# Kernel optimization log

Hardware: AMD Instinct MI355X
Metric: run time of the kernel (lower is better)

The kernel has to match this reference:

```python
import jax, jax.numpy as jnp
import numpy as np

N_NODES = 100000
N_EDGES = 1000000
F_IN = 64
F_HID = 64
F_OUT = 2
NUM_GRAPHS = 64


def setup_inputs() -> dict:
    key = jax.random.key(0)
    ks = jax.random.split(key, 8)
    x = jax.random.normal(ks[0], (N_NODES, F_IN), dtype=jnp.float32)
    edge_index = jax.random.randint(ks[1], (2, N_EDGES), 0, N_NODES, dtype=jnp.int32)
    batch = jnp.sort(jax.random.randint(ks[2], (N_NODES,), 0, NUM_GRAPHS, dtype=jnp.int32))
    s1 = 1.0 / np.sqrt(F_IN)
    s2 = 1.0 / np.sqrt(F_HID)
    W1 = jax.random.normal(ks[3], (F_IN, F_HID), dtype=jnp.float32) * s1
    W2 = jax.random.normal(ks[4], (F_HID, F_HID), dtype=jnp.float32) * s2
    W3 = jax.random.normal(ks[5], (F_HID, F_HID), dtype=jnp.float32) * s2
    Wlin = jax.random.normal(ks[6], (F_HID, F_OUT), dtype=jnp.float32) * s2
    return {
        "x": x, "edge_index": edge_index, "batch": batch,
        "W1": W1, "b1": jnp.zeros((F_HID,), jnp.float32),
        "W2": W2, "b2": jnp.zeros((F_HID,), jnp.float32),
        "W3": W3, "b3": jnp.zeros((F_HID,), jnp.float32),
        "Wlin": Wlin, "blin": jnp.zeros((F_OUT,), jnp.float32),
    }


def _gcn_norm(edge_index, n_nodes):
    # add self-loops, compute symmetric D^-1/2 (A+I) D^-1/2 edge weights
    loops = jnp.arange(n_nodes, dtype=edge_index.dtype)
    src = jnp.concatenate([edge_index[0], loops])  # message source j
    dst = jnp.concatenate([edge_index[1], loops])  # aggregation target i
    deg = jax.ops.segment_sum(jnp.ones_like(dst, dtype=jnp.float32), dst,
                              num_segments=n_nodes)
    dinv = jnp.where(deg > 0, jax.lax.rsqrt(deg), 0.0)
    norm = dinv[src] * dinv[dst]  # [E+N]
    return src, dst, norm


def _gcn_conv(h, W, b, src, dst, norm, n_nodes):
    h = h @ W                                    # [N, F] dense transform first (PyG order)
    msg = h[src] * norm[:, None]                 # gather + scale  [E+N, F]
    agg = jax.ops.segment_sum(msg, dst, num_segments=n_nodes)
    return agg + b


def reference(x, edge_index, batch, W1, b1, W2, b2, W3, b3, Wlin, blin):
    n = x.shape[0]
    src, dst, norm = _gcn_norm(edge_index, n)
    h = jax.nn.relu(_gcn_conv(x, W1, b1, src, dst, norm, n))
    h = jax.nn.relu(_gcn_conv(h, W2, b2, src, dst, norm, n))
    h = _gcn_conv(h, W3, b3, src, dst, norm, n)
    # global mean pool over graphs
    sums = jax.ops.segment_sum(h, batch, num_segments=NUM_GRAPHS)        # [G, F]
    cnts = jax.ops.segment_sum(jnp.ones((n,), jnp.float32), batch,
                               num_segments=NUM_GRAPHS)
    pooled = sums / jnp.maximum(cnts, 1.0)[:, None]
    # dropout(p=0.1) is identity in eval mode
    return pooled @ Wlin + blin
```

## Files before the change

kernel.cpp:

```cpp
#include <hip/hip_runtime.h>

#define FDIM 64

typedef unsigned short u16;

__device__ __forceinline__ u16 f2bf(float x) {
    unsigned int u = __float_as_uint(x);
    return (u16)((u + 0x7fff + ((u >> 16) & 1)) >> 16);
}
__device__ __forceinline__ float bf2f(u16 h) {
    return __uint_as_float(((unsigned int)h) << 16);
}
__device__ __forceinline__ float2 up2(unsigned int u) {
    float2 r;
    r.x = __uint_as_float(u << 16);
    r.y = __uint_as_float(u & 0xffff0000u);
    return r;
}


template <bool BF16IN>
__device__ __forceinline__ void mm_tile64(
    const void* __restrict__ ain, const float* __restrict__ bias, int do_relu,
    u16* __restrict__ t, int n, int blk,
    float (*__restrict__ As)[FDIM + 1], float* __restrict__ Ws)
{
    int tid = threadIdx.x;
    int r0 = blk * 64;

    #pragma unroll
    for (int i = 0; i < 4; ++i) {
        int idx = tid + 256 * i;
        int r = idx >> 4;
        int kq = idx & 15;
        float4 v = make_float4(0.f, 0.f, 0.f, 0.f);
        int R = r0 + r;
        if (R < n) {
            if (BF16IN) {
                ushort4 h = ((const ushort4*)ain)[(size_t)R * 16 + kq];
                v.x = bf2f(h.x); v.y = bf2f(h.y); v.z = bf2f(h.z); v.w = bf2f(h.w);
            } else {
                v = ((const float4*)ain)[(size_t)R * 16 + kq];
            }
            if (bias != nullptr) {
                float4 b = ((const float4*)bias)[kq];
                v.x += b.x; v.y += b.y; v.z += b.z; v.w += b.w;
            }
            if (do_relu) {
                v.x = fmaxf(v.x, 0.f); v.y = fmaxf(v.y, 0.f);
                v.z = fmaxf(v.z, 0.f); v.w = fmaxf(v.w, 0.f);
            }
        }
        As[r][kq * 4 + 0] = v.x;
        As[r][kq * 4 + 1] = v.y;
        As[r][kq * 4 + 2] = v.z;
        As[r][kq * 4 + 3] = v.w;
    }
    __syncthreads();

    int rq = tid >> 4;
    int cq = tid & 15;
    float acc[4][4];
    #pragma unroll
    for (int i = 0; i < 4; ++i)
        #pragma unroll
        for (int j = 0; j < 4; ++j) acc[i][j] = 0.f;

    const float4* Ws4 = (const float4*)Ws;
    #pragma unroll 4
    for (int k = 0; k < FDIM; ++k) {
        float4 w = Ws4[k * 16 + cq];
        float a[4];
        #pragma unroll
        for (int i = 0; i < 4; ++i) a[i] = As[rq * 4 + i][k];
        #pragma unroll
        for (int i = 0; i < 4; ++i) {
            acc[i][0] = fmaf(a[i], w.x, acc[i][0]);
            acc[i][1] = fmaf(a[i], w.y, acc[i][1]);
            acc[i][2] = fmaf(a[i], w.z, acc[i][2]);
            acc[i][3] = fmaf(a[i], w.w, acc[i][3]);
        }
    }

    #pragma unroll
    for (int i = 0; i < 4; ++i) {
        int R = r0 + rq * 4 + i;
        if (R < n) {
            ushort4 o;
            o.x = f2bf(acc[i][0]); o.y = f2bf(acc[i][1]);
            o.z = f2bf(acc[i][2]); o.w = f2bf(acc[i][3]);
            ((ushort4*)t)[(size_t)R * 16 + cq] = o;
        }
    }
}

__global__ __launch_bounds__(256) void k_matmul_h(
    const u16* __restrict__ ain, const float* __restrict__ Wm,
    const float* __restrict__ bias, u16* __restrict__ t, int n)
{
    __shared__ float As[64][FDIM + 1];
    __shared__ float Ws[FDIM * FDIM];
    int tid = threadIdx.x;
    #pragma unroll
    for (int i = 0; i < 4; ++i)
        ((float4*)Ws)[tid + 256 * i] = ((const float4*)Wm)[tid + 256 * i];
    mm_tile64<true>(ain, bias, 1, t, n, blockIdx.x, As, Ws);
}


__global__ __launch_bounds__(256) void k_mm_fill(
    const float* __restrict__ x, const float* __restrict__ W1,
    u16* __restrict__ t,
    const int* __restrict__ src, const int* __restrict__ dst,
    int* __restrict__ cnt, int* __restrict__ csr,
    int n, int E, int cap, int mm_blocks, int fill_chunks)
{
    __shared__ float As[64][FDIM + 1];
    __shared__ float Ws[FDIM * FDIM];

    if ((int)blockIdx.x < mm_blocks) {
        int tid = threadIdx.x;
        #pragma unroll
        for (int i = 0; i < 4; ++i)
            ((float4*)Ws)[tid + 256 * i] = ((const float4*)W1)[tid + 256 * i];
        mm_tile64<false>(x, nullptr, 0, t, n, blockIdx.x, As, Ws);
        return;
    }
    int gb = blockIdx.x - mm_blocks;
    int part = blockIdx.x & 7;
    int chunk = gb >> 3;
    int psz = n >> 3;
    int lo = psz * part;
    int hi = (part == 7) ? n : lo + psz;
    int per = (E + fill_chunks - 1) / fill_chunks;
    int e1 = chunk * per + per; if (e1 > E) e1 = E;
    for (int e = chunk * per + threadIdx.x; e < e1; e += 256) {
        int d = dst[e];
        if (d >= lo && d < hi) {
            int p = atomicAdd(&cnt[d], 1);
            if (p < cap)
                __builtin_nontemporal_store(src[e], &csr[(size_t)d * cap + p]);
        }
    }
}


__global__ __launch_bounds__(256) void k_aggregate(
    const int* __restrict__ cnt, const int* __restrict__ csr,
    const u16* __restrict__ t, float* __restrict__ aggf,
    unsigned int* __restrict__ aggh, int outf32, int n, int cap)
{
    int tid = threadIdx.x;
    long long gw = ((long long)blockIdx.x * 256 + tid) >> 6;
    int lane = tid & 63;
    int half = lane >> 5;
    int fp = lane & 31;
    long long il = gw * 2 + half;
    if (il >= n) return;
    int i = (int)il;

    int deg = cnt[i];
    float di = rsqrtf((float)deg + 1.0f);
    int m = deg < cap ? deg : cap;
    int mm32 = m < 32 ? m : 32;

    const unsigned int* tu = (const unsigned int*)t;
    float2 a0 = up2(tu[(size_t)i * 32 + fp]);
    a0.x *= di; a0.y *= di;
    float2 a1 = make_float2(0.f, 0.f);
    float2 a2 = make_float2(0.f, 0.f);
    float2 a3 = make_float2(0.f, 0.f);

    const int* row = csr + (size_t)i * cap;
    int sv = 0; float dvv = 0.f;
    if (fp < mm32) { sv = row[fp]; dvv = rsqrtf((float)cnt[sv] + 1.0f); }

    int base = half << 5;
    int k = 0;
    for (; k + 8 <= mm32; k += 8) {
        int jv[8]; float dj[8]; unsigned int v[8];
        #pragma unroll
        for (int u = 0; u < 8; ++u) {
            jv[u] = __shfl(sv, base + k + u);
            dj[u] = __shfl(dvv, base + k + u);
        }
        #pragma unroll
        for (int u = 0; u < 8; ++u) v[u] = tu[(size_t)jv[u] * 32 + fp];
        float2 x0 = up2(v[0]), x1 = up2(v[1]), x2 = up2(v[2]), x3 = up2(v[3]);
        float2 x4 = up2(v[4]), x5 = up2(v[5]), x6 = up2(v[6]), x7 = up2(v[7]);
        a0.x = fmaf(x0.x, dj[0], a0.x); a0.y = fmaf(x0.y, dj[0], a0.y);
        a1.x = fmaf(x1.x, dj[1], a1.x); a1.y = fmaf(x1.y, dj[1], a1.y);
        a2.x = fmaf(x2.x, dj[2], a2.x); a2.y = fmaf(x2.y, dj[2], a2.y);
        a3.x = fmaf(x3.x, dj[3], a3.x); a3.y = fmaf(x3.y, dj[3], a3.y);
        a0.x = fmaf(x4.x, dj[4], a0.x); a0.y = fmaf(x4.y, dj[4], a0.y);
        a1.x = fmaf(x5.x, dj[5], a1.x); a1.y = fmaf(x5.y, dj[5], a1.y);
        a2.x = fmaf(x6.x, dj[6], a2.x); a2.y = fmaf(x6.y, dj[6], a2.y);
        a3.x = fmaf(x7.x, dj[7], a3.x); a3.y = fmaf(x7.y, dj[7], a3.y);
    }
    if (k + 4 <= mm32) {
        int jv[4]; float dj[4]; unsigned int v[4];
        #pragma unroll
        for (int u = 0; u < 4; ++u) {
            jv[u] = __shfl(sv, base + k + u);
            dj[u] = __shfl(dvv, base + k + u);
        }
        #pragma unroll
        for (int u = 0; u < 4; ++u) v[u] = tu[(size_t)jv[u] * 32 + fp];
        float2 x0 = up2(v[0]), x1 = up2(v[1]), x2 = up2(v[2]), x3 = up2(v[3]);
        a0.x = fmaf(x0.x, dj[0], a0.x); a0.y = fmaf(x0.y, dj[0], a0.y);
        a1.x = fmaf(x1.x, dj[1], a1.x); a1.y = fmaf(x1.y, dj[1], a1.y);
        a2.x = fmaf(x2.x, dj[2], a2.x); a2.y = fmaf(x2.y, dj[2], a2.y);
        a3.x = fmaf(x3.x, dj[3], a3.x); a3.y = fmaf(x3.y, dj[3], a3.y);
        k += 4;
    }
    for (; k < mm32; ++k) {
        int j = __shfl(sv, base + k);
        float dj = __shfl(dvv, base + k);
        float2 xx = up2(tu[(size_t)j * 32 + fp]);
        a0.x = fmaf(xx.x, dj, a0.x); a0.y = fmaf(xx.y, dj, a0.y);
    }
    for (int kk = 32; kk < m; ++kk) {
        int j = row[kk];
        float dj = rsqrtf((float)cnt[j] + 1.0f);
        float2 xx = up2(tu[(size_t)j * 32 + fp]);
        a0.x = fmaf(xx.x, dj, a0.x); a0.y = fmaf(xx.y, dj, a0.y);
    }

    float ox = ((a0.x + a1.x) + (a2.x + a3.x)) * di;
    float oy = ((a0.y + a1.y) + (a2.y + a3.y)) * di;
    if (outf32) {
        ((float2*)aggf)[(size_t)i * 32 + fp] = make_float2(ox, oy);
    } else {
        unsigned int pk = ((unsigned int)f2bf(ox)) | (((unsigned int)f2bf(oy)) << 16);
        aggh[(size_t)i * 32 + fp] = pk;
    }
}


__global__ __launch_bounds__(256) void k_pool1(
    const float* __restrict__ agg, const int* __restrict__ batch,
    float* __restrict__ partial, int n)
{
    int g = blockIdx.x >> 3;
    int part = blockIdx.x & 7;
    int tid = threadIdx.x;

    int lo = 0, hi = n;
    while (lo < hi) { int mid = (lo + hi) >> 1; if (batch[mid] < g) lo = mid + 1; else hi = mid; }
    int start = lo;
    hi = n;
    while (lo < hi) { int mid = (lo + hi) >> 1; if (batch[mid] <= g) lo = mid + 1; else hi = mid; }
    int end = lo;

    int f = tid & 63, r = tid >> 6;
    float s = 0.f;
    for (int i = start + part * 4 + r; i < end; i += 32)
        s += agg[(size_t)i * 64 + f];

    __shared__ float red[4][64];
    red[r][f] = s;
    __syncthreads();
    if (tid < 64)
        partial[((size_t)g * 8 + part) * 64 + tid] =
            red[0][tid] + red[1][tid] + red[2][tid] + red[3][tid];
}

__global__ __launch_bounds__(64) void k_pool2(
    const float* __restrict__ partial, const int* __restrict__ batch,
    const float* __restrict__ b3, const float* __restrict__ Wlin,
    const float* __restrict__ blin, float* __restrict__ out,
    int n, int fout)
{
    int g = blockIdx.x;
    int tid = threadIdx.x;

    int lo = 0, hi = n;
    while (lo < hi) { int mid = (lo + hi) >> 1; if (batch[mid] < g) lo = mid + 1; else hi = mid; }
    int start = lo;
    hi = n;
    while (lo < hi) { int mid = (lo + hi) >> 1; if (batch[mid] <= g) lo = mid + 1; else hi = mid; }
    int cnt = lo - start;

    __shared__ float pooled[64];
    float v = 0.f;
    #pragma unroll
    for (int p = 0; p < 8; ++p) v += partial[((size_t)g * 8 + p) * 64 + tid];
    pooled[tid] = (cnt > 0) ? (v / (float)cnt + b3[tid]) : 0.f;
    __syncthreads();
    if (tid < fout) {
        float o = blin[tid];
        for (int k = 0; k < 64; ++k) o += pooled[k] * Wlin[k * fout + tid];
        out[(size_t)g * fout + tid] = o;
    }
}


extern "C" void kernel_launch(void* const* d_in, const int* in_sizes, int n_in,
                              void* d_out, int out_size, void* d_ws, size_t ws_size,
                              hipStream_t stream) {
    const float* x     = (const float*)d_in[0];
    const int*   ei    = (const int*)d_in[1];
    const int*   batch = (const int*)d_in[2];
    const float* W1 = (const float*)d_in[3];
    const float* b1 = (const float*)d_in[4];
    const float* W2 = (const float*)d_in[5];
    const float* b2 = (const float*)d_in[6];
    const float* W3 = (const float*)d_in[7];
    const float* b3 = (const float*)d_in[8];
    const float* Wl = (const float*)d_in[9];
    const float* bl = (const float*)d_in[10];

    int n = in_sizes[0] / 64;
    int E = in_sizes[1] / 2;
    int fout = in_sizes[10];
    int ngraphs = out_size / fout;

    const int* srcp = ei;
    const int* dstp = ei + E;

    float* ws   = (float*)d_ws;
    float* agg  = ws;
    u16*   t    = (u16*)(agg + (size_t)n * 64);
    float* partial = (float*)(t + (size_t)n * 64);
    int* cnt    = (int*)(partial + 64 * 8 * 64);
    int* csr    = cnt + n;

    size_t fixed = (size_t)n * 64 * 4 + (size_t)n * 64 * 2 +
                   64 * 8 * 64 * 4 + (size_t)n * 4;
    int cap = 64;
    while (cap > 32 && fixed + (size_t)n * cap * 4 > ws_size) cap -= 8;

    int nb_ag = (int)((((long long)(n + 1) / 2) * 64 + 255) / 256);
    int mm_blocks = (((n + 63) / 64 + 7) / 8) * 8;
    int fill_chunks = 128;

    hipMemsetAsync(cnt, 0, (size_t)n * sizeof(int), stream);
    k_mm_fill<<<mm_blocks + 8 * fill_chunks, 256, 0, stream>>>(
        x, W1, t, srcp, dstp, cnt, csr, n, E, cap, mm_blocks, fill_chunks);

    k_aggregate<<<nb_ag, 256, 0, stream>>>(cnt, csr, t, agg, (unsigned int*)agg, 0, n, cap);
    k_matmul_h<<<mm_blocks, 256, 0, stream>>>((const u16*)agg, W2, b1, t, n);
    k_aggregate<<<nb_ag, 256, 0, stream>>>(cnt, csr, t, agg, (unsigned int*)agg, 0, n, cap);
    k_matmul_h<<<mm_blocks, 256, 0, stream>>>((const u16*)agg, W3, b2, t, n);
    k_aggregate<<<nb_ag, 256, 0, stream>>>(cnt, csr, t, agg, (unsigned int*)agg, 1, n, cap);

    k_pool1<<<ngraphs * 8, 256, 0, stream>>>(agg, batch, partial, n);
    k_pool2<<<ngraphs, 64, 0, stream>>>(partial, batch, b3, Wl, bl, (float*)d_out, n, fout);
}
```

Baseline: 297.0 us.

## Aggregate four nodes per wavefront with 16 lanes and 8-byte feature loads

Reworks the GCN aggregation kernel so each 64-lane wavefront handles four destination nodes, each served by 16 lanes that load four bf16 features (uint2) per gather instead of two. The neighbor list is walked in chunks of 16 with shuffled indices and degrees, replacing the separate slow serial path for neighbors beyond 32. The intent is fewer, wider gather transactions, more nodes in flight, and less lane divergence on high-degree nodes. It also drops the nontemporal hint on CSR stores in the fill kernel, which may change cache behaviour for the later CSR reads.

```diff
diff --git a/kernel.cpp b/kernel.cpp
--- a/kernel.cpp
+++ b/kernel.cpp
@@ -138,8 +138,7 @@
         int d = dst[e];
         if (d >= lo && d < hi) {
             int p = atomicAdd(&cnt[d], 1);
-            if (p < cap)
-                __builtin_nontemporal_store(src[e], &csr[(size_t)d * cap + p]);
+            if (p < cap) csr[(size_t)d * cap + p] = src[e];
         }
     }
 }
@@ -148,91 +147,101 @@
 __global__ __launch_bounds__(256) void k_aggregate(
     const int* __restrict__ cnt, const int* __restrict__ csr,
     const u16* __restrict__ t, float* __restrict__ aggf,
-    unsigned int* __restrict__ aggh, int outf32, int n, int cap)
+    uint2* __restrict__ aggh, int outf32, int n, int cap)
 {
     int tid = threadIdx.x;
     long long gw = ((long long)blockIdx.x * 256 + tid) >> 6;
     int lane = tid & 63;
-    int half = lane >> 5;
-    int fp = lane & 31;
-    long long il = gw * 2 + half;
+    int sub = lane >> 4;
+    int li  = lane & 15;
+    long long il = gw * 4 + sub;
     if (il >= n) return;
     int i = (int)il;
 
     int deg = cnt[i];
     float di = rsqrtf((float)deg + 1.0f);
     int m = deg < cap ? deg : cap;
-    int mm32 = m < 32 ? m : 32;
-
-    const unsigned int* tu = (const unsigned int*)t;
-    float2 a0 = up2(tu[(size_t)i * 32 + fp]);
-    a0.x *= di; a0.y *= di;
-    float2 a1 = make_float2(0.f, 0.f);
-    float2 a2 = make_float2(0.f, 0.f);
-    float2 a3 = make_float2(0.f, 0.f);
+
+    const uint2* tu = (const uint2*)t;
+    uint2 sp = tu[(size_t)i * 16 + li];
+    float2 s0 = up2(sp.x), s1 = up2(sp.y);
+    float4 A0 = make_float4(s0.x * di, s0.y * di, s1.x * di, s1.y * di);
+    float4 A1 = make_float4(0.f, 0.f, 0.f, 0.f);
+    float4 A2 = make_float4(0.f, 0.f, 0.f, 0.f);
+    float4 A3 = make_float4(0.f, 0.f, 0.f, 0.f);
 
     const int* row = csr + (size_t)i * cap;
-    int sv = 0; float dvv = 0.f;
-    if (fp < mm32) { sv = row[fp]; dvv = rsqrtf((float)cnt[sv] + 1.0f); }
-
-    int base = half << 5;
-    int k = 0;
-    for (; k + 8 <= mm32; k += 8) {
-        int jv[8]; float dj[8]; unsigned int v[8];
-        #pragma unroll
-        for (int u = 0; u < 8; ++u) {
-            jv[u] = __shfl(sv, base + k + u);
-            dj[u] = __shfl(dvv, base + k + u);
-        }
-        #pragma unroll
-        for (int u = 0; u < 8; ++u) v[u] = tu[(size_t)jv[u] * 32 + fp];
-        float2 x0 = up2(v[0]), x1 = up2(v[1]), x2 = up2(v[2]), x3 = up2(v[3]);
-        float2 x4 = up2(v[4]), x5 = up2(v[5]), x6 = up2(v[6]), x7 = up2(v[7]);
-        a0.x = fmaf(x0.x, dj[0], a0.x); a0.y = fmaf(x0.y, dj[0], a0.y);
-        a1.x = fmaf(x1.x, dj[1], a1.x); a1.y = fmaf(x1.y, dj[1], a1.y);
-        a2.x = fmaf(x2.x, dj[2], a2.x); a2.y = fmaf(x2.y, dj[2], a2.y);
-        a3.x = fmaf(x3.x, dj[3], a3.x); a3.y = fmaf(x3.y, dj[3], a3.y);
-        a0.x = fmaf(x4.x, dj[4], a0.x); a0.y = fmaf(x4.y, dj[4], a0.y);
-        a1.x = fmaf(x5.x, dj[5], a1.x); a1.y = fmaf(x5.y, dj[5], a1.y);
-        a2.x = fmaf(x6.x, dj[6], a2.x); a2.y = fmaf(x6.y, dj[6], a2.y);
-        a3.x = fmaf(x7.x, dj[7], a3.x); a3.y = fmaf(x7.y, dj[7], a3.y);
-    }
-    if (k + 4 <= mm32) {
-        int jv[4]; float dj[4]; unsigned int v[4];
-        #pragma unroll
-        for (int u = 0; u < 4; ++u) {
-            jv[u] = __shfl(sv, base + k + u);
-            dj[u] = __shfl(dvv, base + k + u);
-        }
-        #pragma unroll
-        for (int u = 0; u < 4; ++u) v[u] = tu[(size_t)jv[u] * 32 + fp];
-        float2 x0 = up2(v[0]), x1 = up2(v[1]), x2 = up2(v[2]), x3 = up2(v[3]);
-        a0.x = fmaf(x0.x, dj[0], a0.x); a0.y = fmaf(x0.y, dj[0], a0.y);
-        a1.x = fmaf(x1.x, dj[1], a1.x); a1.y = fmaf(x1.y, dj[1], a1.y);
-        a2.x = fmaf(x2.x, dj[2], a2.x); a2.y = fmaf(x2.y, dj[2], a2.y);
-        a3.x = fmaf(x3.x, dj[3], a3.x); a3.y = fmaf(x3.y, dj[3], a3.y);
-        k += 4;
-    }
-    for (; k < mm32; ++k) {
-        int j = __shfl(sv, base + k);
-        float dj = __shfl(dvv, base + k);
-        float2 xx = up2(tu[(size_t)j * 32 + fp]);
-        a0.x = fmaf(xx.x, dj, a0.x); a0.y = fmaf(xx.y, dj, a0.y);
-    }
-    for (int kk = 32; kk < m; ++kk) {
-        int j = row[kk];
-        float dj = rsqrtf((float)cnt[j] + 1.0f);
-        float2 xx = up2(tu[(size_t)j * 32 + fp]);
-        a0.x = fmaf(xx.x, dj, a0.x); a0.y = fmaf(xx.y, dj, a0.y);
-    }
-
-    float ox = ((a0.x + a1.x) + (a2.x + a3.x)) * di;
-    float oy = ((a0.y + a1.y) + (a2.y + a3.y)) * di;
+    int nbase = sub << 4;
+
+    for (int c0 = 0; c0 < m; c0 += 16) {
+        int cm = m - c0; if (cm > 16) cm = 16;
+        int sv = 0; float dvv = 0.f;
+        if (li < cm) { sv = row[c0 + li]; dvv = rsqrtf((float)cnt[sv] + 1.0f); }
+        int k = 0;
+        for (; k + 8 <= cm; k += 8) {
+            int jv[8]; float dj[8]; uint2 v[8];
+            #pragma unroll
+            for (int u = 0; u < 8; ++u) {
+                jv[u] = __shfl(sv, nbase + k + u);
+                dj[u] = __shfl(dvv, nbase + k + u);
+            }
+            #pragma unroll
+            for (int u = 0; u < 8; ++u) v[u] = tu[(size_t)jv[u] * 16 + li];
+            #pragma unroll
+            for (int u = 0; u < 8; ++u) {
+                float2 x0 = up2(v[u].x), x1 = up2(v[u].y);
+                float4* Ap = (u & 3) == 0 ? &A0 : (u & 3) == 1 ? &A1 :
+                             (u & 3) == 2 ? &A2 : &A3;
+                Ap->x = fmaf(x0.x, dj[u], Ap->x);
+                Ap->y = fmaf(x0.y, dj[u], Ap->y);
+                Ap->z = fmaf(x1.x, dj[u], Ap->z);
+                Ap->w = fmaf(x1.y, dj[u], Ap->w);
+            }
+        }
+        if (k + 4 <= cm) {
+            int jv[4]; float dj[4]; uint2 v[4];
+            #pragma unroll
+            for (int u = 0; u < 4; ++u) {
+                jv[u] = __shfl(sv, nbase + k + u);
+                dj[u] = __shfl(dvv, nbase + k + u);
+            }
+            #pragma unroll
+            for (int u = 0; u < 4; ++u) v[u] = tu[(size_t)jv[u] * 16 + li];
+            #pragma unroll
+            for (int u = 0; u < 4; ++u) {
+                float2 x0 = up2(v[u].x), x1 = up2(v[u].y);
+                float4* Ap = u == 0 ? &A0 : u == 1 ? &A1 : u == 2 ? &A2 : &A3;
+                Ap->x = fmaf(x0.x, dj[u], Ap->x);
+                Ap->y = fmaf(x0.y, dj[u], Ap->y);
+                Ap->z = fmaf(x1.x, dj[u], Ap->z);
+                Ap->w = fmaf(x1.y, dj[u], Ap->w);
+            }
+            k += 4;
+        }
+        for (; k < cm; ++k) {
+            int j = __shfl(sv, nbase + k);
+            float dj = __shfl(dvv, nbase + k);
+            uint2 vv = tu[(size_t)j * 16 + li];
+            float2 x0 = up2(vv.x), x1 = up2(vv.y);
+            A0.x = fmaf(x0.x, dj, A0.x);
+            A0.y = fmaf(x0.y, dj, A0.y);
+            A0.z = fmaf(x1.x, dj, A0.z);
+            A0.w = fmaf(x1.y, dj, A0.w);
+        }
+    }
+
+    float4 O;
+    O.x = ((A0.x + A1.x) + (A2.x + A3.x)) * di;
+    O.y = ((A0.y + A1.y) + (A2.y + A3.y)) * di;
+    O.z = ((A0.z + A1.z) + (A2.z + A3.z)) * di;
+    O.w = ((A0.w + A1.w) + (A2.w + A3.w)) * di;
     if (outf32) {
-        ((float2*)aggf)[(size_t)i * 32 + fp] = make_float2(ox, oy);
+        ((float4*)aggf)[(size_t)i * 16 + li] = O;
     } else {
-        unsigned int pk = ((unsigned int)f2bf(ox)) | (((unsigned int)f2bf(oy)) << 16);
-        aggh[(size_t)i * 32 + fp] = pk;
+        uint2 pk;
+        pk.x = ((unsigned int)f2bf(O.x)) | (((unsigned int)f2bf(O.y)) << 16);
+        pk.y = ((unsigned int)f2bf(O.z)) | (((unsigned int)f2bf(O.w)) << 16);
+        aggh[(size_t)i * 16 + li] = pk;
     }
 }
 
@@ -330,7 +339,7 @@
     int cap = 64;
     while (cap > 32 && fixed + (size_t)n * cap * 4 > ws_size) cap -= 8;
 
-    int nb_ag = (int)((((long long)(n + 1) / 2) * 64 + 255) / 256);
+    int nb_ag = (int)((((long long)(n + 3) / 4) * 64 + 255) / 256);
     int mm_blocks = (((n + 63) / 64 + 7) / 8) * 8;
     int fill_chunks = 128;
 
@@ -338,11 +347,11 @@
     k_mm_fill<<<mm_blocks + 8 * fill_chunks, 256, 0, stream>>>(
         x, W1, t, srcp, dstp, cnt, csr, n, E, cap, mm_blocks, fill_chunks);
 
-    k_aggregate<<<nb_ag, 256, 0, stream>>>(cnt, csr, t, agg, (unsigned int*)agg, 0, n, cap);
+    k_aggregate<<<nb_ag, 256, 0, stream>>>(cnt, csr, t, agg, (uint2*)agg, 0, n, cap);
     k_matmul_h<<<mm_blocks, 256, 0, stream>>>((const u16*)agg, W2, b1, t, n);
-    k_aggregate<<<nb_ag, 256, 0, stream>>>(cnt, csr, t, agg, (unsigned int*)agg, 0, n, cap);
+    k_aggregate<<<nb_ag, 256, 0, stream>>>(cnt, csr, t, agg, (uint2*)agg, 0, n, cap);
     k_matmul_h<<<mm_blocks, 256, 0, stream>>>((const u16*)agg, W3, b2, t, n);
-    k_aggregate<<<nb_ag, 256, 0, stream>>>(cnt, csr, t, agg, (unsigned int*)agg, 1, n, cap);
+    k_aggregate<<<nb_ag, 256, 0, stream>>>(cnt, csr, t, agg, (uint2*)agg, 1, n, cap);
 
     k_pool1<<<ngraphs * 8, 256, 0, stream>>>(agg, batch, partial, n);
     k_pool2<<<ngraphs, 64, 0, stream>>>(partial, batch, b3, Wl, bl, (float*)d_out, n, fout);
```

Measured after the change: 291.5 us. Within noise of the previous version (-1.8%).
